# Performance work log

Hardware: AMD Instinct MI355X
Metric: run time of the kernel (lower is better)

Reference implementation:

```python
import jax, jax.numpy as jnp
import numpy as np
import math

DIM = 768
FFN_DIM = 4 * DIM
EPS = 1e-5

def layer_norm(x, gamma, beta):
    mu = jnp.mean(x, axis=-1, keepdims=True)
    var = jnp.var(x, axis=-1, keepdims=True)
    return (x - mu) * jax.lax.rsqrt(var + EPS) * gamma + beta

def setup_inputs() -> dict:
    key = jax.random.key(0)
    ks = jax.random.split(key, 8)
    b, n, d = 8, 2048, DIM
    s = 1.0 / math.sqrt(d)
    x = jax.random.normal(ks[0], (b, n, d), dtype=jnp.float32)
    Wq = jax.random.normal(ks[1], (d, d), dtype=jnp.float32) * s
    Wk = jax.random.normal(ks[2], (d, d), dtype=jnp.float32) * s
    Wv = jax.random.normal(ks[3], (d, d), dtype=jnp.float32) * s
    W1 = jax.random.normal(ks[4], (d, FFN_DIM), dtype=jnp.float32) * s
    b1 = jnp.zeros((FFN_DIM,), dtype=jnp.float32)
    W2 = jax.random.normal(ks[5], (FFN_DIM, d), dtype=jnp.float32) * (1.0 / math.sqrt(FFN_DIM))
    b2 = jnp.zeros((d,), dtype=jnp.float32)
    g1 = jnp.ones((d,), dtype=jnp.float32); be1 = jnp.zeros((d,), dtype=jnp.float32)
    g2 = jnp.ones((d,), dtype=jnp.float32); be2 = jnp.zeros((d,), dtype=jnp.float32)
    return {"x": x, "Wq": Wq, "Wk": Wk, "Wv": Wv, "ln1_g": g1, "ln1_b": be1,
            "W1": W1, "b1": b1, "W2": W2, "b2": b2, "ln2_g": g2, "ln2_b": be2}

def reference(x, Wq, Wk, Wv, ln1_g, ln1_b, W1, b1, W2, b2, ln2_g, ln2_b):
    # Self-attention (single head, full dim; dropout in eval mode => identity)
    Q = jnp.einsum('bnd,de->bne', x, Wq)
    K = jnp.einsum('bnd,de->bne', x, Wk)
    V = jnp.einsum('bnd,de->bne', x, Wv)
    scores = jnp.einsum('bnd,bmd->bnm', Q, K) / math.sqrt(DIM)  # [b,n,n]
    attn = jax.nn.softmax(scores, axis=-1)
    O = jnp.einsum('bnm,bmd->bnd', attn, V)
    h = layer_norm(x + O, ln1_g, ln1_b)
    # FFN with exact GELU (torch nn.GELU default)
    hidden = jax.nn.gelu(jnp.einsum('bnd,df->bnf', h, W1) + b1, approximate=False)
    out = jnp.einsum('bnf,fd->bnd', hidden, W2) + b2
    return layer_norm(h + out, ln2_g, ln2_b)
```

## Files before the change

kernel.cpp:

```cpp
#include <hip/hip_runtime.h>
#include <hip/hip_bf16.h>
#include <math.h>

using u16 = unsigned short;
typedef __bf16 bf16x8 __attribute__((ext_vector_type(8)));
typedef float f32x4 __attribute__((ext_vector_type(4)));
typedef u16 u16x8 __attribute__((ext_vector_type(8)));

__device__ __forceinline__ u16 f2b(float f) {
  union { float f; unsigned u; } c; c.f = f;
  unsigned r = c.u + 0x7fffu + ((c.u >> 16) & 1u);
  return (u16)(r >> 16);
}
__device__ __forceinline__ float b2f(u16 h) {
  union { unsigned u; float f; } c; c.u = ((unsigned)h) << 16;
  return c.f;
}

__device__ __forceinline__ float fast_gelu(float t) {
  float y = fminf(1.5957691216f * t + 0.07135481283f * t * t * t, 80.f);
  float e = __expf(y);
  return t * e * (1.0f / (e + 1.0f));
}

#define EPI_BF16 0
#define EPI_BF16_SCALE 1
#define EPI_GELU_BIAS 2
#define EPI_F32_BIAS 3
#define EPI_BF16_BIAS 4

#define GLDS16(src, dst)                                                     \
  __builtin_amdgcn_global_load_lds(                                          \
      (const __attribute__((address_space(1))) void*)(src),                  \
      (__attribute__((address_space(3))) void*)(dst), 16, 0, 0)

__device__ __forceinline__ int xswz(int o, int n) {
  int q = n >> 3, r = n & 7, x = o & 7, i = o >> 3;
  return (x < r ? x * (q + 1) : r * (q + 1) + (x - r) * q) + i;
}

template <int EPI>
__device__ __forceinline__ void epi_store(
    void* Cg, const float* bias, float v, long long off, int ccol, float scale)
{
  if (EPI == EPI_BF16) {
    ((u16*)Cg)[off] = f2b(v);
  } else if (EPI == EPI_BF16_SCALE) {
    ((u16*)Cg)[off] = f2b(v * scale);
  } else if (EPI == EPI_GELU_BIAS) {
    ((u16*)Cg)[off] = f2b(fast_gelu(v + bias[ccol]));
  } else if (EPI == EPI_F32_BIAS) {
    ((float*)Cg)[off] = v + bias[ccol];
  } else {
    ((u16*)Cg)[off] = f2b(v + bias[ccol]);
  }
}

template <int EPI>
__global__ __launch_bounds__(256, 2) void gemm128(
    const u16* __restrict__ Ag, const u16* __restrict__ Bg,
    void* __restrict__ Cg, const float* __restrict__ bias,
    int nbx, int K, float scale, int lda, int ldb, int ldc,
    long long sAz, long long sBz, long long sCz)
{
  __shared__ __align__(16) u16 lds[32768];

  const int tid = threadIdx.x;
  const int wave = tid >> 6, lane = tid & 63;
  const int wr = wave >> 1, wc = wave & 1;
  const int id = xswz(blockIdx.x, gridDim.x);
  const int bx = id % nbx, by = id / nbx;
  const int m0 = by * 128, n0 = bx * 128;
  const long long z = blockIdx.z;
  const u16* A = Ag + z * sAz + (long long)m0 * lda;
  const u16* B = Bg + z * sBz + (long long)n0 * ldb;

  const int rA = wave * 32 + (lane >> 2);
  const int slot = (lane & 3) ^ ((rA >> 1) & 3);
  const u16* a0 = A + (long long)rA * lda + slot * 8;
  const u16* a1 = a0 + (long long)16 * lda;
  const u16* b0 = B + (long long)rA * ldb + slot * 8;
  const u16* b1 = b0 + (long long)16 * ldb;
  const int d0 = wave * 32 * 32;
  const int d1 = (wave * 32 + 16) * 32;

  int offA[4], offB[4];
#pragma unroll
  for (int f = 0; f < 4; ++f) {
    int ra = wr * 64 + f * 16 + (lane & 15);
    int ba = ra * 64 + ((lane >> 4) << 4);
    offA[f] = ba ^ (((ba >> 7) & 3) << 4);
    int rb = wc * 64 + f * 16 + (lane & 15);
    int bb = rb * 64 + ((lane >> 4) << 4);
    offB[f] = bb ^ (((bb >> 7) & 3) << 4);
  }

  f32x4 acc[4][4];
#pragma unroll
  for (int m = 0; m < 4; ++m)
#pragma unroll
    for (int n = 0; n < 4; ++n) acc[m][n] = f32x4{0.f, 0.f, 0.f, 0.f};

  const char* ldsc = (const char*)lds;
  const int NT = K >> 6;

  GLDS16(a0, lds + 0 * 4096 + d0);  GLDS16(a1, lds + 0 * 4096 + d1);
  GLDS16(b0, lds + 2 * 4096 + d0);  GLDS16(b1, lds + 2 * 4096 + d1);
  GLDS16(a0 + 32, lds + 1 * 4096 + d0);  GLDS16(a1 + 32, lds + 1 * 4096 + d1);
  GLDS16(b0 + 32, lds + 3 * 4096 + d0);  GLDS16(b1 + 32, lds + 3 * 4096 + d1);
  asm volatile("s_waitcnt vmcnt(4)" ::: "memory");
  asm volatile("s_barrier" ::: "memory");

  for (int t = 0; t < NT; ++t) {
    const int buf = t & 1, nb = buf ^ 1;
    const int kc = (t + 1 < NT) ? ((t + 1) << 6) : 0;
    const char* pA0 = ldsc + (buf * 4 + 0) * 8192;
    const char* pA1 = ldsc + (buf * 4 + 1) * 8192;
    const char* pB0 = ldsc + (buf * 4 + 2) * 8192;
    const char* pB1 = ldsc + (buf * 4 + 3) * 8192;
    u16* q = lds + nb * 4 * 4096;

    bf16x8 Af[4], Bf[4];

    GLDS16(a0 + kc, q + 0 * 4096 + d0);  GLDS16(a1 + kc, q + 0 * 4096 + d1);
    GLDS16(b0 + kc, q + 2 * 4096 + d0);  GLDS16(b1 + kc, q + 2 * 4096 + d1);
#pragma unroll
    for (int m = 0; m < 4; ++m) Af[m] = *(const bf16x8*)(pA0 + offA[m]);
#pragma unroll
    for (int n = 0; n < 4; ++n) Bf[n] = *(const bf16x8*)(pB0 + offB[n]);
    asm volatile("s_barrier" ::: "memory");
    __builtin_amdgcn_s_setprio(1);
#pragma unroll
    for (int m = 0; m < 4; ++m)
#pragma unroll
      for (int n = 0; n < 4; ++n)
        acc[m][n] = __builtin_amdgcn_mfma_f32_16x16x32_bf16(Af[m], Bf[n], acc[m][n], 0, 0, 0);
    __builtin_amdgcn_s_setprio(0);
    asm volatile("s_waitcnt vmcnt(4)" ::: "memory");
    asm volatile("s_barrier" ::: "memory");

    GLDS16(a0 + kc + 32, q + 1 * 4096 + d0);  GLDS16(a1 + kc + 32, q + 1 * 4096 + d1);
    GLDS16(b0 + kc + 32, q + 3 * 4096 + d0);  GLDS16(b1 + kc + 32, q + 3 * 4096 + d1);
#pragma unroll
    for (int m = 0; m < 4; ++m) Af[m] = *(const bf16x8*)(pA1 + offA[m]);
#pragma unroll
    for (int n = 0; n < 4; ++n) Bf[n] = *(const bf16x8*)(pB1 + offB[n]);
    asm volatile("s_barrier" ::: "memory");
    __builtin_amdgcn_s_setprio(1);
#pragma unroll
    for (int m = 0; m < 4; ++m)
#pragma unroll
      for (int n = 0; n < 4; ++n)
        acc[m][n] = __builtin_amdgcn_mfma_f32_16x16x32_bf16(Af[m], Bf[n], acc[m][n], 0, 0, 0);
    __builtin_amdgcn_s_setprio(0);
    asm volatile("s_waitcnt vmcnt(4)" ::: "memory");
    asm volatile("s_barrier" ::: "memory");
  }

#pragma unroll
  for (int mf = 0; mf < 4; ++mf) {
#pragma unroll
    for (int nf = 0; nf < 4; ++nf) {
      const int crow = m0 + wr * 64 + mf * 16 + (lane >> 4) * 4;
      const int ccol = n0 + wc * 64 + nf * 16 + (lane & 15);
#pragma unroll
      for (int j = 0; j < 4; ++j) {
        const long long off = (long long)(crow + j) * ldc + ccol + z * sCz;
        epi_store<EPI>(Cg, bias, acc[mf][nf][j], off, ccol, scale);
      }
    }
  }
}

__global__ __launch_bounds__(256) void cast_f32_bf16(
    const float* __restrict__ x, u16* __restrict__ y, long long n4)
{
  const long long i = (long long)blockIdx.x * 256 + threadIdx.x;
  if (i >= n4) return;
  const float4 v = ((const float4*)x)[i];
  ushort4 o;
  o.x = f2b(v.x); o.y = f2b(v.y); o.z = f2b(v.z); o.w = f2b(v.w);
  ((ushort4*)y)[i] = o;
}

template <bool SRC_BF16>
__global__ __launch_bounds__(256) void transpose_cast(
    const void* __restrict__ srcv, u16* __restrict__ dst, int R, int C, int ldsrc,
    long long szSrc, long long szDst)
{
  __shared__ float tile[32][33];
  const long long zs = (long long)blockIdx.z * szSrc;
  const long long zd = (long long)blockIdx.z * szDst;
  const int c0 = blockIdx.x * 32, r0 = blockIdx.y * 32;
  const int tx = threadIdx.x & 31, ty = threadIdx.x >> 5;
#pragma unroll
  for (int i = 0; i < 4; ++i) {
    const int r = r0 + ty + i * 8;
    float v;
    if (SRC_BF16) v = b2f(((const u16*)srcv)[zs + (long long)r * ldsrc + c0 + tx]);
    else          v = ((const float*)srcv)[zs + (long long)r * ldsrc + c0 + tx];
    tile[ty + i * 8][tx] = v;
  }
  __syncthreads();
#pragma unroll
  for (int i = 0; i < 4; ++i) {
    const int c = c0 + ty + i * 8;
    dst[zd + (long long)c * R + r0 + tx] = f2b(tile[tx][ty + i * 8]);
  }
}

__global__ __launch_bounds__(256) void softmax_rows(
    u16* __restrict__ S, int ncol)
{
  __shared__ float red[8];
  const long long row = blockIdx.x;
  u16* s = S + row * ncol;
  const int t = threadIdx.x;

  const u16x8 u = *(const u16x8*)&s[t * 8];
  float v[8];
#pragma unroll
  for (int j = 0; j < 8; ++j) v[j] = b2f(u[j]);

  float mx = v[0];
#pragma unroll
  for (int j = 1; j < 8; ++j) mx = fmaxf(mx, v[j]);
  for (int o = 32; o; o >>= 1) mx = fmaxf(mx, __shfl_xor(mx, o));
  if ((t & 63) == 0) red[t >> 6] = mx;
  __syncthreads();
  mx = fmaxf(fmaxf(red[0], red[1]), fmaxf(red[2], red[3]));

  float sum = 0.f;
#pragma unroll
  for (int j = 0; j < 8; ++j) { v[j] = __expf(v[j] - mx); sum += v[j]; }
  for (int o = 32; o; o >>= 1) sum += __shfl_xor(sum, o);
  if ((t & 63) == 0) red[4 + (t >> 6)] = sum;
  __syncthreads();
  sum = red[4] + red[5] + red[6] + red[7];

  const float inv = 1.0f / sum;
  u16x8 o8;
#pragma unroll
  for (int j = 0; j < 8; ++j) o8[j] = f2b(v[j] * inv);
  *(u16x8*)&s[t * 8] = o8;
}

__global__ __launch_bounds__(256) void ln1_kernel(
    const float* __restrict__ x, const u16* __restrict__ O,
    const float* __restrict__ g, const float* __restrict__ be,
    u16* __restrict__ h)
{
  __shared__ float red[8];
  const long long row = blockIdx.x;
  const float* xr = x + row * 768;
  const u16* orow = O + row * 768;
  const int t = threadIdx.x, base = t * 3;

  float v[3];
#pragma unroll
  for (int j = 0; j < 3; ++j) v[j] = xr[base + j] + b2f(orow[base + j]);
  float s = v[0] + v[1] + v[2];
  float ss = v[0] * v[0] + v[1] * v[1] + v[2] * v[2];
  for (int o = 32; o; o >>= 1) { s += __shfl_xor(s, o); ss += __shfl_xor(ss, o); }
  if ((t & 63) == 0) { red[t >> 6] = s; red[4 + (t >> 6)] = ss; }
  __syncthreads();
  s = red[0] + red[1] + red[2] + red[3];
  ss = red[4] + red[5] + red[6] + red[7];
  const float mu = s * (1.0f / 768.0f);
  const float var = ss * (1.0f / 768.0f) - mu * mu;
  const float inv = rsqrtf(var + 1e-5f);
#pragma unroll
  for (int j = 0; j < 3; ++j) {
    const float o = (v[j] - mu) * inv * g[base + j] + be[base + j];
    h[row * 768 + base + j] = f2b(o);
  }
}

__global__ __launch_bounds__(256) void ln2_kernel(
    const u16* __restrict__ h, const u16* __restrict__ ob,
    const float* __restrict__ g, const float* __restrict__ be,
    float* __restrict__ y)
{
  __shared__ float red[8];
  const long long row = blockIdx.x;
  const u16* hr = h + row * 768;
  const u16* orow = ob + row * 768;
  const int t = threadIdx.x, base = t * 3;

  float v[3];
#pragma unroll
  for (int j = 0; j < 3; ++j) v[j] = b2f(hr[base + j]) + b2f(orow[base + j]);
  float s = v[0] + v[1] + v[2];
  float ss = v[0] * v[0] + v[1] * v[1] + v[2] * v[2];
  for (int o = 32; o; o >>= 1) { s += __shfl_xor(s, o); ss += __shfl_xor(ss, o); }
  if ((t & 63) == 0) { red[t >> 6] = s; red[4 + (t >> 6)] = ss; }
  __syncthreads();
  s = red[0] + red[1] + red[2] + red[3];
  ss = red[4] + red[5] + red[6] + red[7];
  const float mu = s * (1.0f / 768.0f);
  const float var = ss * (1.0f / 768.0f) - mu * mu;
  const float inv = rsqrtf(var + 1e-5f);
#pragma unroll
  for (int j = 0; j < 3; ++j) {
    y[row * 768 + base + j] = (v[j] - mu) * inv * g[base + j] + be[base + j];
  }
}

extern "C" void kernel_launch(void* const* d_in, const int* in_sizes, int n_in,
                              void* d_out, int out_size, void* d_ws, size_t ws_size,
                              hipStream_t stream)
{
  const int Bb = 8, Nn = 2048, D = 768, F = 3072, E = 1536;
  const int M = Bb * Nn;
  const long long MD = (long long)M * D;

  const float* x   = (const float*)d_in[0];
  const float* Wq  = (const float*)d_in[1];
  const float* Wk  = (const float*)d_in[2];
  const float* Wv  = (const float*)d_in[3];
  const float* g1  = (const float*)d_in[4];
  const float* be1 = (const float*)d_in[5];
  const float* W1  = (const float*)d_in[6];
  const float* b1  = (const float*)d_in[7];
  const float* W2  = (const float*)d_in[8];
  const float* b2  = (const float*)d_in[9];
  const float* g2  = (const float*)d_in[10];
  const float* be2 = (const float*)d_in[11];

  u16* xb   = (u16*)d_out;
  u16* wqkt = xb + MD;
  u16* wvt  = wqkt + (size_t)E * D;

  char* w = (char*)d_ws;
  size_t off = 0;
  auto alloc = [&](size_t bytes) { void* p = w + off; off += bytes; return p; };
  u16* w1t = (u16*)alloc((size_t)F * D * 2);
  u16* w2t = (u16*)alloc((size_t)D * F * 2);
  u16* hb  = (u16*)alloc((size_t)MD * 2);
  u16* qk  = (u16*)alloc((size_t)M * E * 2);
  u16* Vt  = (u16*)alloc((size_t)Bb * D * Nn * 2);
  u16* S   = (u16*)alloc((size_t)Bb * Nn * Nn * 2);
  u16* O   = (u16*)alloc((size_t)MD * 2);
  u16* hidden = qk;
  u16* outf   = qk + (size_t)M * F;

  const dim3 tcb(256);
  const float scl = 0.03608439182435161f;

  cast_f32_bf16<<<(unsigned)(MD / 4 / 256), 256, 0, stream>>>(x, xb, MD / 4);
  transpose_cast<false><<<dim3(D / 32, D / 32, 1), tcb, 0, stream>>>(Wq, wqkt, D, D, D, 0, 0);
  transpose_cast<false><<<dim3(D / 32, D / 32, 1), tcb, 0, stream>>>(Wk, wqkt + D * D, D, D, D, 0, 0);
  transpose_cast<false><<<dim3(D / 32, D / 32, 1), tcb, 0, stream>>>(Wv, wvt, D, D, D, 0, 0);
  transpose_cast<false><<<dim3(F / 32, D / 32, 1), tcb, 0, stream>>>(W1, w1t, D, F, F, 0, 0);
  transpose_cast<false><<<dim3(D / 32, F / 32, 1), tcb, 0, stream>>>(W2, w2t, F, D, D, 0, 0);

  gemm128<EPI_BF16><<<dim3(12 * 128, 1, 1), 256, 0, stream>>>(
      xb, wqkt, qk, nullptr, 12, D, 1.f, D, D, E, 0, 0, 0);

  gemm128<EPI_BF16><<<dim3(16 * 6, 1, Bb), 256, 0, stream>>>(
      wvt, xb, Vt, nullptr, 16, D, 1.f, D, D, Nn,
      0, (long long)Nn * D, (long long)D * Nn);

  gemm128<EPI_BF16_SCALE><<<dim3(16 * 16, 1, Bb), 256, 0, stream>>>(
      qk, qk + D, S, nullptr, 16, D, scl, E, E, Nn,
      (long long)Nn * E, (long long)Nn * E, (long long)Nn * Nn);

  softmax_rows<<<M, 256, 0, stream>>>(S, Nn);

  gemm128<EPI_BF16><<<dim3(6 * 16, 1, Bb), 256, 0, stream>>>(
      S, Vt, O, nullptr, 6, Nn, 1.f, Nn, Nn, D,
      (long long)Nn * Nn, (long long)D * Nn, (long long)Nn * D);

  ln1_kernel<<<M, 256, 0, stream>>>(x, O, g1, be1, hb);

  gemm128<EPI_GELU_BIAS><<<dim3(24 * 128, 1, 1), 256, 0, stream>>>(
      hb, w1t, hidden, b1, 24, D, 1.f, D, D, F, 0, 0, 0);

  gemm128<EPI_BF16_BIAS><<<dim3(6 * 128, 1, 1), 256, 0, stream>>>(
      hidden, w2t, outf, b2, 6, F, 1.f, F, F, D, 0, 0, 0);

  ln2_kernel<<<M, 256, 0, stream>>>(hb, outf, g2, be2, (float*)d_out);
}
```

Baseline: 525.1 us.

## Fuse softmax into QK GEMM epilogue and widen GEMM tiles to 128x256

The QK^T GEMM epilogue now computes exp(score*scale) directly, without subtracting the row max, stores it in bf16, and atomically accumulates row sums. The standalone softmax kernel is removed, and the normalisation by the row sum moves into ln1. Separately, every GEMM now uses 512-thread blocks with 128x256 tiles, a K-step of 32 and a simpler double buffer. LN1 also reads residual x from its bf16 copy. Dropping the max subtraction risks overflow or precision loss for large scores, and the atomics and the extra zeroing kernel add some overhead.

```diff
diff --git a/kernel.cpp b/kernel.cpp
--- a/kernel.cpp
+++ b/kernel.cpp
@@ -24,9 +24,8 @@
 }
 
 #define EPI_BF16 0
-#define EPI_BF16_SCALE 1
+#define EPI_EXP_SUM 1
 #define EPI_GELU_BIAS 2
-#define EPI_F32_BIAS 3
 #define EPI_BF16_BIAS 4
 
 #define GLDS16(src, dst)                                                     \
@@ -45,44 +44,42 @@
 {
   if (EPI == EPI_BF16) {
     ((u16*)Cg)[off] = f2b(v);
-  } else if (EPI == EPI_BF16_SCALE) {
-    ((u16*)Cg)[off] = f2b(v * scale);
   } else if (EPI == EPI_GELU_BIAS) {
     ((u16*)Cg)[off] = f2b(fast_gelu(v + bias[ccol]));
-  } else if (EPI == EPI_F32_BIAS) {
-    ((float*)Cg)[off] = v + bias[ccol];
   } else {
     ((u16*)Cg)[off] = f2b(v + bias[ccol]);
   }
 }
 
 template <int EPI>
-__global__ __launch_bounds__(256, 2) void gemm128(
+__global__ __launch_bounds__(512, 4) void gemmW(
     const u16* __restrict__ Ag, const u16* __restrict__ Bg,
     void* __restrict__ Cg, const float* __restrict__ bias,
     int nbx, int K, float scale, int lda, int ldb, int ldc,
-    long long sAz, long long sBz, long long sCz)
-{
-  __shared__ __align__(16) u16 lds[32768];
+    long long sAz, long long sBz, long long sCz,
+    float* __restrict__ lsum, int lzs)
+{
+  __shared__ __align__(16) u16 lds[24576];
 
   const int tid = threadIdx.x;
   const int wave = tid >> 6, lane = tid & 63;
-  const int wr = wave >> 1, wc = wave & 1;
+  const int wr = wave >> 2, wc = wave & 3;
   const int id = xswz(blockIdx.x, gridDim.x);
   const int bx = id % nbx, by = id / nbx;
-  const int m0 = by * 128, n0 = bx * 128;
+  const int m0 = by * 128, n0 = bx * 256;
   const long long z = blockIdx.z;
   const u16* A = Ag + z * sAz + (long long)m0 * lda;
   const u16* B = Bg + z * sBz + (long long)n0 * ldb;
 
-  const int rA = wave * 32 + (lane >> 2);
-  const int slot = (lane & 3) ^ ((rA >> 1) & 3);
-  const u16* a0 = A + (long long)rA * lda + slot * 8;
-  const u16* a1 = a0 + (long long)16 * lda;
-  const u16* b0 = B + (long long)rA * ldb + slot * 8;
-  const u16* b1 = b0 + (long long)16 * ldb;
-  const int d0 = wave * 32 * 32;
-  const int d1 = (wave * 32 + 16) * 32;
+  const int rA = wave * 16 + (lane >> 2);
+  const int sA = (lane & 3) ^ ((rA >> 1) & 3);
+  const u16* pa = A + (long long)rA * lda + sA * 8;
+  const int rB = wave * 32 + (lane >> 2);
+  const int sB = (lane & 3) ^ ((rB >> 1) & 3);
+  const u16* pb0 = B + (long long)rB * ldb + sB * 8;
+  const u16* pb1 = pb0 + (long long)16 * ldb;
+  const int dA = wave * 512;
+  const int dB0 = wave * 1024, dB1 = wave * 1024 + 512;
 
   int offA[4], offB[4];
 #pragma unroll
@@ -102,33 +99,29 @@
     for (int n = 0; n < 4; ++n) acc[m][n] = f32x4{0.f, 0.f, 0.f, 0.f};
 
   const char* ldsc = (const char*)lds;
-  const int NT = K >> 6;
-
-  GLDS16(a0, lds + 0 * 4096 + d0);  GLDS16(a1, lds + 0 * 4096 + d1);
-  GLDS16(b0, lds + 2 * 4096 + d0);  GLDS16(b1, lds + 2 * 4096 + d1);
-  GLDS16(a0 + 32, lds + 1 * 4096 + d0);  GLDS16(a1 + 32, lds + 1 * 4096 + d1);
-  GLDS16(b0 + 32, lds + 3 * 4096 + d0);  GLDS16(b1 + 32, lds + 3 * 4096 + d1);
-  asm volatile("s_waitcnt vmcnt(4)" ::: "memory");
+  const int NT = K >> 5;
+
+  GLDS16(pa, lds + dA);
+  GLDS16(pb0, lds + 4096 + dB0);
+  GLDS16(pb1, lds + 4096 + dB1);
+  asm volatile("s_waitcnt vmcnt(0)" ::: "memory");
   asm volatile("s_barrier" ::: "memory");
 
   for (int t = 0; t < NT; ++t) {
-    const int buf = t & 1, nb = buf ^ 1;
-    const int kc = (t + 1 < NT) ? ((t + 1) << 6) : 0;
-    const char* pA0 = ldsc + (buf * 4 + 0) * 8192;
-    const char* pA1 = ldsc + (buf * 4 + 1) * 8192;
-    const char* pB0 = ldsc + (buf * 4 + 2) * 8192;
-    const char* pB1 = ldsc + (buf * 4 + 3) * 8192;
-    u16* q = lds + nb * 4 * 4096;
+    const int kc = (t + 1 < NT ? t + 1 : 0) << 5;
+    const char* cur = ldsc + (t & 1) * 24576;
+    u16* nxt = lds + ((t & 1) ^ 1) * 12288;
+
+    GLDS16(pa + kc, nxt + dA);
+    GLDS16(pb0 + kc, nxt + 4096 + dB0);
+    GLDS16(pb1 + kc, nxt + 4096 + dB1);
 
     bf16x8 Af[4], Bf[4];
-
-    GLDS16(a0 + kc, q + 0 * 4096 + d0);  GLDS16(a1 + kc, q + 0 * 4096 + d1);
-    GLDS16(b0 + kc, q + 2 * 4096 + d0);  GLDS16(b1 + kc, q + 2 * 4096 + d1);
-#pragma unroll
-    for (int m = 0; m < 4; ++m) Af[m] = *(const bf16x8*)(pA0 + offA[m]);
-#pragma unroll
-    for (int n = 0; n < 4; ++n) Bf[n] = *(const bf16x8*)(pB0 + offB[n]);
-    asm volatile("s_barrier" ::: "memory");
+#pragma unroll
+    for (int f = 0; f < 4; ++f) {
+      Af[f] = *(const bf16x8*)(cur + offA[f]);
+      Bf[f] = *(const bf16x8*)(cur + 8192 + offB[f]);
+    }
     __builtin_amdgcn_s_setprio(1);
 #pragma unroll
     for (int m = 0; m < 4; ++m)
@@ -136,40 +129,56 @@
       for (int n = 0; n < 4; ++n)
         acc[m][n] = __builtin_amdgcn_mfma_f32_16x16x32_bf16(Af[m], Bf[n], acc[m][n], 0, 0, 0);
     __builtin_amdgcn_s_setprio(0);
-    asm volatile("s_waitcnt vmcnt(4)" ::: "memory");
+
+    asm volatile("s_waitcnt vmcnt(0)" ::: "memory");
     asm volatile("s_barrier" ::: "memory");
-
-    GLDS16(a0 + kc + 32, q + 1 * 4096 + d0);  GLDS16(a1 + kc + 32, q + 1 * 4096 + d1);
-    GLDS16(b0 + kc + 32, q + 3 * 4096 + d0);  GLDS16(b1 + kc + 32, q + 3 * 4096 + d1);
-#pragma unroll
-    for (int m = 0; m < 4; ++m) Af[m] = *(const bf16x8*)(pA1 + offA[m]);
-#pragma unroll
-    for (int n = 0; n < 4; ++n) Bf[n] = *(const bf16x8*)(pB1 + offB[n]);
-    asm volatile("s_barrier" ::: "memory");
-    __builtin_amdgcn_s_setprio(1);
-#pragma unroll
-    for (int m = 0; m < 4; ++m)
-#pragma unroll
-      for (int n = 0; n < 4; ++n)
-        acc[m][n] = __builtin_amdgcn_mfma_f32_16x16x32_bf16(Af[m], Bf[n], acc[m][n], 0, 0, 0);
-    __builtin_amdgcn_s_setprio(0);
-    asm volatile("s_waitcnt vmcnt(4)" ::: "memory");
-    asm volatile("s_barrier" ::: "memory");
-  }
-
-#pragma unroll
-  for (int mf = 0; mf < 4; ++mf) {
-#pragma unroll
-    for (int nf = 0; nf < 4; ++nf) {
+  }
+
+  if (EPI == EPI_EXP_SUM) {
+#pragma unroll
+    for (int mf = 0; mf < 4; ++mf) {
       const int crow = m0 + wr * 64 + mf * 16 + (lane >> 4) * 4;
-      const int ccol = n0 + wc * 64 + nf * 16 + (lane & 15);
+      float part[4] = {0.f, 0.f, 0.f, 0.f};
+#pragma unroll
+      for (int nf = 0; nf < 4; ++nf) {
+        const int ccol = n0 + wc * 64 + nf * 16 + (lane & 15);
+#pragma unroll
+        for (int j = 0; j < 4; ++j) {
+          const float p = __expf(fminf(acc[mf][nf][j] * scale, 60.f));
+          const u16 ub = f2b(p);
+          ((u16*)Cg)[(long long)(crow + j) * ldc + ccol + z * sCz] = ub;
+          part[j] += b2f(ub);
+        }
+      }
 #pragma unroll
       for (int j = 0; j < 4; ++j) {
-        const long long off = (long long)(crow + j) * ldc + ccol + z * sCz;
-        epi_store<EPI>(Cg, bias, acc[mf][nf][j], off, ccol, scale);
+        float s = part[j];
+        s += __shfl_xor(s, 1); s += __shfl_xor(s, 2);
+        s += __shfl_xor(s, 4); s += __shfl_xor(s, 8);
+        if ((lane & 15) == 0)
+          atomicAdd(&lsum[(long long)z * lzs + crow + j], s);
       }
     }
-  }
+  } else {
+#pragma unroll
+    for (int mf = 0; mf < 4; ++mf) {
+#pragma unroll
+      for (int nf = 0; nf < 4; ++nf) {
+        const int crow = m0 + wr * 64 + mf * 16 + (lane >> 4) * 4;
+        const int ccol = n0 + wc * 64 + nf * 16 + (lane & 15);
+#pragma unroll
+        for (int j = 0; j < 4; ++j) {
+          const long long off = (long long)(crow + j) * ldc + ccol + z * sCz;
+          epi_store<EPI>(Cg, bias, acc[mf][nf][j], off, ccol, scale);
+        }
+      }
+    }
+  }
+}
+
+__global__ __launch_bounds__(256) void zero_f32(float* __restrict__ p, int n) {
+  const int i = blockIdx.x * 256 + threadIdx.x;
+  if (i < n) p[i] = 0.f;
 }
 
 __global__ __launch_bounds__(256) void cast_f32_bf16(
@@ -209,56 +218,22 @@
   }
 }
 
-__global__ __launch_bounds__(256) void softmax_rows(
-    u16* __restrict__ S, int ncol)
+__global__ __launch_bounds__(256) void ln1_kernel(
+    const u16* __restrict__ xb, const u16* __restrict__ O,
+    const float* __restrict__ l,
+    const float* __restrict__ g, const float* __restrict__ be,
+    u16* __restrict__ h)
 {
   __shared__ float red[8];
   const long long row = blockIdx.x;
-  u16* s = S + row * ncol;
-  const int t = threadIdx.x;
-
-  const u16x8 u = *(const u16x8*)&s[t * 8];
-  float v[8];
-#pragma unroll
-  for (int j = 0; j < 8; ++j) v[j] = b2f(u[j]);
-
-  float mx = v[0];
-#pragma unroll
-  for (int j = 1; j < 8; ++j) mx = fmaxf(mx, v[j]);
-  for (int o = 32; o; o >>= 1) mx = fmaxf(mx, __shfl_xor(mx, o));
-  if ((t & 63) == 0) red[t >> 6] = mx;
-  __syncthreads();
-  mx = fmaxf(fmaxf(red[0], red[1]), fmaxf(red[2], red[3]));
-
-  float sum = 0.f;
-#pragma unroll
-  for (int j = 0; j < 8; ++j) { v[j] = __expf(v[j] - mx); sum += v[j]; }
-  for (int o = 32; o; o >>= 1) sum += __shfl_xor(sum, o);
-  if ((t & 63) == 0) red[4 + (t >> 6)] = sum;
-  __syncthreads();
-  sum = red[4] + red[5] + red[6] + red[7];
-
-  const float inv = 1.0f / sum;
-  u16x8 o8;
-#pragma unroll
-  for (int j = 0; j < 8; ++j) o8[j] = f2b(v[j] * inv);
-  *(u16x8*)&s[t * 8] = o8;
-}
-
-__global__ __launch_bounds__(256) void ln1_kernel(
-    const float* __restrict__ x, const u16* __restrict__ O,
-    const float* __restrict__ g, const float* __restrict__ be,
-    u16* __restrict__ h)
-{
-  __shared__ float red[8];
-  const long long row = blockIdx.x;
-  const float* xr = x + row * 768;
+  const u16* xr = xb + row * 768;
   const u16* orow = O + row * 768;
+  const float invl = 1.0f / l[row];
   const int t = threadIdx.x, base = t * 3;
 
   float v[3];
 #pragma unroll
-  for (int j = 0; j < 3; ++j) v[j] = xr[base + j] + b2f(orow[base + j]);
+  for (int j = 0; j < 3; ++j) v[j] = b2f(xr[base + j]) + b2f(orow[base + j]) * invl;
   float s = v[0] + v[1] + v[2];
   float ss = v[0] * v[0] + v[1] * v[1] + v[2] * v[2];
   for (int o = 32; o; o >>= 1) { s += __shfl_xor(s, o); ss += __shfl_xor(ss, o); }
@@ -337,6 +312,7 @@
   u16* w1t = (u16*)alloc((size_t)F * D * 2);
   u16* w2t = (u16*)alloc((size_t)D * F * 2);
   u16* hb  = (u16*)alloc((size_t)MD * 2);
+  float* lrow = (float*)alloc((size_t)M * 4);
   u16* qk  = (u16*)alloc((size_t)M * E * 2);
   u16* Vt  = (u16*)alloc((size_t)Bb * D * Nn * 2);
   u16* S   = (u16*)alloc((size_t)Bb * Nn * Nn * 2);
@@ -347,6 +323,7 @@
   const dim3 tcb(256);
   const float scl = 0.03608439182435161f;
 
+  zero_f32<<<M / 256, 256, 0, stream>>>(lrow, M);
   cast_f32_bf16<<<(unsigned)(MD / 4 / 256), 256, 0, stream>>>(x, xb, MD / 4);
   transpose_cast<false><<<dim3(D / 32, D / 32, 1), tcb, 0, stream>>>(Wq, wqkt, D, D, D, 0, 0);
   transpose_cast<false><<<dim3(D / 32, D / 32, 1), tcb, 0, stream>>>(Wk, wqkt + D * D, D, D, D, 0, 0);
@@ -354,30 +331,28 @@
   transpose_cast<false><<<dim3(F / 32, D / 32, 1), tcb, 0, stream>>>(W1, w1t, D, F, F, 0, 0);
   transpose_cast<false><<<dim3(D / 32, F / 32, 1), tcb, 0, stream>>>(W2, w2t, F, D, D, 0, 0);
 
-  gemm128<EPI_BF16><<<dim3(12 * 128, 1, 1), 256, 0, stream>>>(
-      xb, wqkt, qk, nullptr, 12, D, 1.f, D, D, E, 0, 0, 0);
-
-  gemm128<EPI_BF16><<<dim3(16 * 6, 1, Bb), 256, 0, stream>>>(
-      wvt, xb, Vt, nullptr, 16, D, 1.f, D, D, Nn,
-      0, (long long)Nn * D, (long long)D * Nn);
-
-  gemm128<EPI_BF16_SCALE><<<dim3(16 * 16, 1, Bb), 256, 0, stream>>>(
-      qk, qk + D, S, nullptr, 16, D, scl, E, E, Nn,
-      (long long)Nn * E, (long long)Nn * E, (long long)Nn * Nn);
-
-  softmax_rows<<<M, 256, 0, stream>>>(S, Nn);
-
-  gemm128<EPI_BF16><<<dim3(6 * 16, 1, Bb), 256, 0, stream>>>(
-      S, Vt, O, nullptr, 6, Nn, 1.f, Nn, Nn, D,
-      (long long)Nn * Nn, (long long)D * Nn, (long long)Nn * D);
-
-  ln1_kernel<<<M, 256, 0, stream>>>(x, O, g1, be1, hb);
-
-  gemm128<EPI_GELU_BIAS><<<dim3(24 * 128, 1, 1), 256, 0, stream>>>(
-      hb, w1t, hidden, b1, 24, D, 1.f, D, D, F, 0, 0, 0);
-
-  gemm128<EPI_BF16_BIAS><<<dim3(6 * 128, 1, 1), 256, 0, stream>>>(
-      hidden, w2t, outf, b2, 6, F, 1.f, F, F, D, 0, 0, 0);
+  gemmW<EPI_BF16><<<dim3(6 * 128, 1, 1), 512, 0, stream>>>(
+      xb, wqkt, qk, nullptr, 6, D, 1.f, D, D, E, 0, 0, 0, nullptr, 0);
+
+  gemmW<EPI_BF16><<<dim3(8 * 6, 1, Bb), 512, 0, stream>>>(
+      wvt, xb, Vt, nullptr, 8, D, 1.f, D, D, Nn,
+      0, (long long)Nn * D, (long long)D * Nn, nullptr, 0);
+
+  gemmW<EPI_EXP_SUM><<<dim3(8 * 16, 1, Bb), 512, 0, stream>>>(
+      qk, qk + D, S, nullptr, 8, D, scl, E, E, Nn,
+      (long long)Nn * E, (long long)Nn * E, (long long)Nn * Nn, lrow, Nn);
+
+  gemmW<EPI_BF16><<<dim3(3 * 16, 1, Bb), 512, 0, stream>>>(
+      S, Vt, O, nullptr, 3, Nn, 1.f, Nn, Nn, D,
+      (long long)Nn * Nn, (long long)D * Nn, (long long)Nn * D, nullptr, 0);
+
+  ln1_kernel<<<M, 256, 0, stream>>>(xb, O, lrow, g1, be1, hb);
+
+  gemmW<EPI_GELU_BIAS><<<dim3(12 * 128, 1, 1), 512, 0, stream>>>(
+      hb, w1t, hidden, b1, 12, D, 1.f, D, D, F, 0, 0, 0, nullptr, 0);
+
+  gemmW<EPI_BF16_BIAS><<<dim3(3 * 128, 1, 1), 512, 0, stream>>>(
+      hidden, w2t, outf, b2, 3, F, 1.f, F, F, D, 0, 0, 0, nullptr, 0);
 
   ln2_kernel<<<M, 256, 0, stream>>>(hb, outf, g2, be2, (float*)d_out);
 }
```

After: 470.3 us (median of 2 runs). 10.4% less time.
